# Kernel tuning notes

Hardware: AMD Instinct MI355X
Metric: run time of the kernel (lower is better)

Reference implementation:

```python
import jax, jax.numpy as jnp
import numpy as np

# ---- static configuration (matches init_kwargs) ----
B, C, H, W = 32, 16, 128, 128
T_MIN, T_MAX, RES = 0.0, 1.0, 64
GH, GW = 2 * H - 1, 2 * W - 1              # vertex-mode cubical grid (gudhi all_cells)
SCALE = (RES - 1) / (T_MAX - T_MIN)

# Cell (i,j) in the (GH,GW) grid has corner vertices (i//2..(i+1)//2, j//2..(j+1)//2).
_i = np.arange(GH); _j = np.arange(GW)
I0, I1 = _i // 2, (_i + 1) // 2
J0, J1 = _j // 2, (_j + 1) // 2
_DIM = (_i % 2)[:, None] + (_j % 2)[None, :]          # 0=vertex, 1=edge, 2=square
SIGN = jnp.asarray(np.where(_DIM % 2 == 0, 1.0, -1.0), jnp.float32)  # (-1)**dim


def _cells(x):
    """x: [B,C,H,W] vertex values -> (corners [4,B,C,GH,GW], F [B,C,GH,GW]).
    Lower-star filtration: a cell's value is the max over its vertices."""
    c00 = x[..., I0[:, None], J0[None, :]]
    c01 = x[..., I0[:, None], J1[None, :]]
    c10 = x[..., I1[:, None], J0[None, :]]
    c11 = x[..., I1[:, None], J1[None, :]]
    corners = jnp.stack([c00, c01, c10, c11])
    return corners, corners.max(axis=0)


def setup_inputs() -> dict:
    key = jax.random.key(0)
    x = jax.random.uniform(key, (B, C, H, W), dtype=jnp.float32)
    return {"x": x}


def reference(x):
    """Euler characteristic curve of the sublevel cubical complex. Returns [B,C,RES]."""
    _, F = _cells(x)                                  # cell filtrations
    # bin index t = max(ceil((filt - t_min)*scale), 0); cells with filt > t_max skipped
    t = jnp.clip(jnp.ceil((F - T_MIN) * SCALE).astype(jnp.int32), 0, RES - 1)
    vals = SIGN * (F <= T_MAX).astype(jnp.float32)    # (-1)**dim masked
    bc, N = B * C, GH * GW
    idx = jnp.arange(bc, dtype=jnp.int32)[:, None] * RES + t.reshape(bc, N)
    hist = jnp.zeros(bc * RES, jnp.float32).at[idx.reshape(-1)].add(
        jnp.broadcast_to(vals, (B, C, GH, GW)).reshape(-1))
    return jnp.cumsum(hist.reshape(B, C, RES), axis=-1)
```

## Files before the change

### kernel.cpp

```cpp
#include <hip/hip_runtime.h>


#define HH 128
#define WW 128
#define RESB 64
#define NT 512
#define RPT 8
#define BC 512

__global__ __launch_bounds__(NT, 6) void ecc_fused(const float* __restrict__ X,
                                                   float* __restrict__ out) {
    __shared__ int hist[RESB * 32];
    const int bc = blockIdx.x;
    const int tid = threadIdx.x;
    const int lnb = (tid & 31) << 2;
    const float* __restrict__ x = X + (size_t)bc * (HH * WW);

    ((int4*)hist)[tid] = make_int4(0, 0, 0, 0);
    __syncthreads();

    auto binqa = [lnb](float F) {
        return ((int)ceilf(F * 63.0f) << 7) + lnb;
    };
    char* const hb = (char*)hist;

    const int col4 = tid & 31;
    const int rg = tid >> 5;
    const int r0 = rg * RPT;
    const int c0 = col4 * 4;
    const int cR = (col4 < 31) ? c0 + 4 : WW - 1;

    int u[5], v[5], w[5];
    {
        const float4 a = *(const float4*)(x + r0 * WW + c0);
        const float aR = x[r0 * WW + cR];
        u[0] = binqa(a.x); u[1] = binqa(a.y); u[2] = binqa(a.z); u[3] = binqa(a.w); u[4] = binqa(aR);
        const float4 b = *(const float4*)(x + (r0 + 1) * WW + c0);
        const float bR = x[(r0 + 1) * WW + cR];
        v[0] = binqa(b.x); v[1] = binqa(b.y); v[2] = binqa(b.z); v[3] = binqa(b.w); v[4] = binqa(bR);
    }

#pragma unroll
    for (int dr = 0; dr < RPT; ++dr) {
        const int hD = (dr < RPT - 1) ? 1 : ((rg < 15) ? 1 : 0);
        float4 p4; float pR;
        if (dr < RPT - 1) {
            const int rn = (r0 + dr + 2 < HH) ? r0 + dr + 2 : HH - 1;
            p4 = *(const float4*)(x + rn * WW + c0);
            pR = x[rn * WW + cR];
        }
#pragma unroll
        for (int k = 0; k < 4; ++k) {
            const int hR = (k < 3) ? 1 : ((col4 < 31) ? 1 : 0);
            const int u00 = u[k];
            const int bh  = max(u00, u[k + 1]);
            const int bvv = max(u00, v[k]);
            const int bf  = max(bh, max(v[k], v[k + 1]));
            atomicAdd((int*)(hb + u00), 1);
            atomicAdd((int*)(hb + bh),  -hR);
            atomicAdd((int*)(hb + bvv), -hD);
            atomicAdd((int*)(hb + bf),  hR & hD);
        }
        if (dr < RPT - 1) {
            w[0] = binqa(p4.x); w[1] = binqa(p4.y); w[2] = binqa(p4.z); w[3] = binqa(p4.w); w[4] = binqa(pR);
#pragma unroll
            for (int k = 0; k < 5; ++k) { u[k] = v[k]; v[k] = w[k]; }
        }
    }
    __syncthreads();

    const int bin = tid & 63;
    const int q = tid >> 6;
    int ssum = 0;
#pragma unroll
    for (int k = 0; k < 4; ++k) {
        ssum += hist[(bin << 5) + ((q * 4 + bin + k) & 31)];
    }
    __syncthreads();
    hist[tid] = ssum;
    __syncthreads();
    if (tid < RESB) {
        int vv = 0;
#pragma unroll
        for (int qq = 0; qq < 8; ++qq) vv += hist[qq * 64 + tid];
#pragma unroll
        for (int d = 1; d < 64; d <<= 1) {
            const int up = __shfl_up(vv, d, 64);
            if (tid >= d) vv += up;
        }
        out[bc * RESB + tid] = (float)vv;
    }
}

extern "C" void kernel_launch(void* const* d_in, const int* in_sizes, int n_in,
                              void* d_out, int out_size, void* d_ws, size_t ws_size,
                              hipStream_t stream) {
    const float* x = (const float*)d_in[0];
    float* out = (float*)d_out;
    ecc_fused<<<BC, NT, 0, stream>>>(x, out);
}
```

Before: 11.54 us.

## Assign each cell's Euler contribution to its argmax vertex, one atomic per pixel

Replaces the four shared-memory atomics per pixel (vertex, two edges, square) with one atomic per pixel. Each cell's sign is credited to the vertex that attains its max, with ties broken by strict and non-strict comparisons. Each thread now loads a 3x6 neighbourhood with left and right halo columns and computes the combined weight with float comparisons. Launch bounds occupancy drops from 6 to 4 blocks to allow more registers. This cuts LDS atomic traffic about fourfold, at the cost of more compares, an extra halo load and possibly lower occupancy.

```diff
diff --git a/kernel.cpp b/kernel.cpp
--- a/kernel.cpp
+++ b/kernel.cpp
@@ -8,7 +8,7 @@
 #define RPT 8
 #define BC 512
 
-__global__ __launch_bounds__(NT, 6) void ecc_fused(const float* __restrict__ X,
+__global__ __launch_bounds__(NT, 4) void ecc_fused(const float* __restrict__ X,
                                                    float* __restrict__ out) {
     __shared__ int hist[RESB * 32];
     const int bc = blockIdx.x;
@@ -19,54 +19,65 @@
     ((int4*)hist)[tid] = make_int4(0, 0, 0, 0);
     __syncthreads();
 
+    char* const hb = (char*)hist;
     auto binqa = [lnb](float F) {
         return ((int)ceilf(F * 63.0f) << 7) + lnb;
     };
-    char* const hb = (char*)hist;
 
     const int col4 = tid & 31;
     const int rg = tid >> 5;
     const int r0 = rg * RPT;
     const int c0 = col4 * 4;
+    const int cL = (col4 > 0) ? c0 - 1 : 0;
     const int cR = (col4 < 31) ? c0 + 4 : WW - 1;
 
-    int u[5], v[5], w[5];
-    {
-        const float4 a = *(const float4*)(x + r0 * WW + c0);
-        const float aR = x[r0 * WW + cR];
-        u[0] = binqa(a.x); u[1] = binqa(a.y); u[2] = binqa(a.z); u[3] = binqa(a.w); u[4] = binqa(aR);
-        const float4 b = *(const float4*)(x + (r0 + 1) * WW + c0);
-        const float bR = x[(r0 + 1) * WW + cR];
-        v[0] = binqa(b.x); v[1] = binqa(b.y); v[2] = binqa(b.z); v[3] = binqa(b.w); v[4] = binqa(bR);
+    float U[6], M[6], D[6];
+#define LOADROW(rr_, row_)                                                   \
+    {                                                                        \
+        const int rr = ((rr_) < 0) ? 0 : (((rr_) > HH - 1) ? HH - 1 : (rr_)); \
+        const float* rp = x + rr * WW;                                       \
+        const float4 a = *(const float4*)(rp + c0);                          \
+        (row_)[1] = a.x; (row_)[2] = a.y; (row_)[3] = a.z; (row_)[4] = a.w;  \
+        (row_)[0] = rp[cL];                                                  \
+        (row_)[5] = rp[cR];                                                  \
     }
+    LOADROW(r0 - 1, U)
+    LOADROW(r0, M)
+    LOADROW(r0 + 1, D)
+
+    const int hl0 = (col4 > 0) ? 1 : 0;
+    const int hr3 = (col4 < 31) ? 1 : 0;
+    const int hU0 = (r0 > 0) ? 1 : 0;
+    const int hD7 = (rg < 15) ? 1 : 0;
 
 #pragma unroll
     for (int dr = 0; dr < RPT; ++dr) {
-        const int hD = (dr < RPT - 1) ? 1 : ((rg < 15) ? 1 : 0);
-        float4 p4; float pR;
-        if (dr < RPT - 1) {
-            const int rn = (r0 + dr + 2 < HH) ? r0 + dr + 2 : HH - 1;
-            p4 = *(const float4*)(x + rn * WW + c0);
-            pR = x[rn * WW + cR];
-        }
+        const int hU = (dr > 0) ? 1 : hU0;
+        const int hD = (dr < RPT - 1) ? 1 : hD7;
+        float P[6];
+        if (dr < RPT - 1) { LOADROW(r0 + dr + 2, P) }
 #pragma unroll
         for (int k = 0; k < 4; ++k) {
-            const int hR = (k < 3) ? 1 : ((col4 < 31) ? 1 : 0);
-            const int u00 = u[k];
-            const int bh  = max(u00, u[k + 1]);
-            const int bvv = max(u00, v[k]);
-            const int bf  = max(bh, max(v[k], v[k + 1]));
-            atomicAdd((int*)(hb + u00), 1);
-            atomicAdd((int*)(hb + bh),  -hR);
-            atomicAdd((int*)(hb + bvv), -hD);
-            atomicAdd((int*)(hb + bf),  hR & hD);
+            const int hl = (k > 0) ? 1 : hl0;
+            const int hr = (k < 3) ? 1 : hr3;
+            const float xv = M[k + 1];
+            const int pL = hl & (M[k] <= xv ? 1 : 0);
+            const int pR = hr & (M[k + 2] < xv ? 1 : 0);
+            const int pU = hU & (U[k + 1] <= xv ? 1 : 0);
+            const int pD = hD & (D[k + 1] < xv ? 1 : 0);
+            const int w = 1 - pL - pR - pU - pD
+                + (pU & pL & (U[k] <= xv ? 1 : 0))
+                + (pU & pR & (U[k + 2] <= xv ? 1 : 0))
+                + (pD & pL & (D[k] < xv ? 1 : 0))
+                + (pD & pR & (D[k + 2] < xv ? 1 : 0));
+            atomicAdd((int*)(hb + binqa(xv)), w);
         }
         if (dr < RPT - 1) {
-            w[0] = binqa(p4.x); w[1] = binqa(p4.y); w[2] = binqa(p4.z); w[3] = binqa(p4.w); w[4] = binqa(pR);
 #pragma unroll
-            for (int k = 0; k < 5; ++k) { u[k] = v[k]; v[k] = w[k]; }
+            for (int t = 0; t < 6; ++t) { U[t] = M[t]; M[t] = D[t]; D[t] = P[t]; }
         }
     }
+#undef LOADROW
     __syncthreads();
 
     const int bin = tid & 63;
```

After: 14.59 us. 1.26x slower.
